# Kernel tuning notes

Measured on AMD Instinct MI355X. Metric: run time of the kernel, lower is better.

The kernel has to match this reference:

```python
import jax, jax.numpy as jnp
import numpy as np

N = 10000   # nodes
E = 160000  # edges (before self-loops)
IN = 77     # input feature dim
H = 4       # heads (layers 1,2)
C = 128     # per-head out channels


def setup_inputs() -> dict:
    key = jax.random.key(0)
    ks = jax.random.split(key, 16)
    p = lambda k, shape: (jax.random.normal(k, shape, jnp.float32) * 0.1)
    z = lambda n: jnp.zeros((n,), jnp.float32)
    return {
        "x": jax.random.normal(ks[0], (N, IN), jnp.float32),
        "edge_index": jax.random.randint(ks[1], (2, E), 0, N),
        # layer 1: 77 -> H*C
        "Wl1": p(ks[2], (H * C, IN)), "bl1": z(H * C),
        "Wr1": p(ks[3], (H * C, IN)), "br1": z(H * C),
        "att1": p(ks[4], (H, C)), "b1": z(H * C),
        # layer 2: H*C -> H*C
        "Wl2": p(ks[5], (H * C, H * C)), "bl2": z(H * C),
        "Wr2": p(ks[6], (H * C, H * C)), "br2": z(H * C),
        "att2": p(ks[7], (H, C)), "b2": z(H * C),
        # layer 3: H*C -> C (1 head)
        "Wl3": p(ks[8], (C, H * C)), "bl3": z(C),
        "Wr3": p(ks[9], (C, H * C)), "br3": z(C),
        "att3": p(ks[10], (1, C)), "b3": z(C),
    }


def _gatv2_layer(x, src, dst, Wl, bl, Wr, br, att, bias, heads, outc):
    """PyG GATv2Conv (eval mode, self-loops already in src/dst, concat=True)."""
    n = x.shape[0]
    xl = (x @ Wl.T + bl).reshape(n, heads, outc)  # source transform
    xr = (x @ Wr.T + br).reshape(n, heads, outc)  # target transform
    # edge-wise score: a^T LeakyReLU(xl[src] + xr[dst])
    e = jax.nn.leaky_relu(xl[src] + xr[dst], negative_slope=0.2)  # [E,H,C]
    logits = jnp.einsum('ehc,hc->eh', e, att)                      # [E,H]
    # segment softmax over edges grouped by destination node
    m = jax.lax.stop_gradient(jax.ops.segment_max(logits, dst, num_segments=n))
    ev = jnp.exp(logits - m[dst])
    denom = jax.ops.segment_sum(ev, dst, num_segments=n)
    alpha = ev / (denom[dst] + 1e-16)                              # [E,H]
    # scatter-add weighted messages
    out = jax.ops.segment_sum(xl[src] * alpha[:, :, None], dst, num_segments=n)
    return out.reshape(n, heads * outc) + bias


def reference(x, edge_index, Wl1, bl1, Wr1, br1, att1, b1,
              Wl2, bl2, Wr2, br2, att2, b2,
              Wl3, bl3, Wr3, br3, att3, b3):
    n = x.shape[0]
    loop = jnp.arange(n)
    src = jnp.concatenate([edge_index[0], loop])  # add self-loops (PyG default)
    dst = jnp.concatenate([edge_index[1], loop])
    h = jax.nn.elu(_gatv2_layer(x, src, dst, Wl1, bl1, Wr1, br1, att1, b1, H, C))
    h = jax.nn.elu(_gatv2_layer(h, src, dst, Wl2, bl2, Wr2, br2, att2, b2, H, C))
    return _gatv2_layer(h, src, dst, Wl3, bl3, Wr3, br3, att3, b3, 1, C)
```

## Files before the change

kernel.cpp:

```cpp
#include <hip/hip_runtime.h>
#include <hip/hip_bf16.h>
#include <math.h>

typedef __attribute__((ext_vector_type(8))) short short8;
typedef __attribute__((ext_vector_type(4))) float f32x4;
typedef __attribute__((ext_vector_type(2))) float f32x2;
typedef __attribute__((ext_vector_type(4))) unsigned int u32x4;

__device__ __forceinline__ float bf2f(unsigned short u) {
  union { unsigned int i; float f; } x; x.i = ((unsigned int)u) << 16; return x.f;
}

__device__ __forceinline__ f32x2 pk_add(f32x2 a, f32x2 b) {
  f32x2 d; asm("v_pk_add_f32 %0, %1, %2" : "=v"(d) : "v"(a), "v"(b)); return d;
}
__device__ __forceinline__ f32x2 pk_fma(f32x2 a, f32x2 b, f32x2 c) {
  f32x2 d; asm("v_pk_fma_f32 %0, %1, %2, %3" : "=v"(d) : "v"(a), "v"(b), "v"(c)); return d;
}
__device__ __forceinline__ f32x2 pk_abs(f32x2 a) {
  union { f32x2 f; unsigned int u[2]; } x; x.f = a;
  x.u[0] &= 0x7fffffffu; x.u[1] &= 0x7fffffffu;
  return x.f;
}
__device__ __forceinline__ f32x2 unpk(unsigned int w) {
  union { f32x2 f; unsigned int u[2]; } x;
  x.u[0] = w << 16;
  x.u[1] = w & 0xffff0000u;
  return x.f;
}

template <int CTRL>
__device__ __forceinline__ float dpp_add(float x) {
  int y = __builtin_amdgcn_update_dpp(0, __builtin_bit_cast(int, x), CTRL, 0xF, 0xF, true);
  return x + __builtin_bit_cast(float, y);
}
__device__ __forceinline__ float row16_sum(float p) {
  p = dpp_add<0xB1>(p);
  p = dpp_add<0x4E>(p);
  p = dpp_add<0x124>(p);
  p = dpp_add<0x128>(p);
  return p;
}

__device__ __forceinline__ void load_lds16(const void* g, void* l) {
  __builtin_amdgcn_global_load_lds(
      (const __attribute__((address_space(1))) unsigned int*)g,
      (__attribute__((address_space(3))) unsigned int*)l, 16, 0, 0);
}

__global__ __launch_bounds__(256) void gemm_mfma(
    const __hip_bfloat16* __restrict__ A, const __hip_bfloat16* __restrict__ B,
    const float* __restrict__ bl, const float* __restrict__ br, int halfN,
    __hip_bfloat16* __restrict__ out, int M, int K, int Nout) {
  __shared__ __hip_bfloat16 As[128 * 32];
  __shared__ __hip_bfloat16 Bs[128 * 32];
  int t = threadIdx.x;
  int w = t >> 6, l = t & 63;
  int lr = l & 15, lh = l >> 4;
  int wr = w >> 1, wc = w & 1;
  int m0 = blockIdx.y * 128, n0 = blockIdx.x * 128;
  f32x4 acc[4][4] = {};
  int nk = K >> 5;
  for (int ks = 0; ks < nk; ++ks) {
    int k0 = ks << 5;
#pragma unroll
    for (int p = 0; p < 2; ++p) {
      int c = p * 256 + t;
      int row = c >> 2, sub = c & 3;
      int gm = m0 + row; if (gm >= M) gm = M - 1;
      const __hip_bfloat16* gsrc = A + (size_t)gm * K + k0 + sub * 8;
      char* ldst = (char*)As + (size_t)(p * 256 + w * 64) * 16;
      load_lds16(gsrc, ldst);
    }
#pragma unroll
    for (int p = 0; p < 2; ++p) {
      int c = p * 256 + t;
      int row = c >> 2, sub = c & 3;
      const __hip_bfloat16* gsrc = B + (size_t)(n0 + row) * K + k0 + sub * 8;
      char* ldst = (char*)Bs + (size_t)(p * 256 + w * 64) * 16;
      load_lds16(gsrc, ldst);
    }
    __syncthreads();
    short8 af[4], bf[4];
#pragma unroll
    for (int mt = 0; mt < 4; ++mt)
      af[mt] = *(const short8*)(As + (size_t)(wr * 64 + mt * 16 + lr) * 32 + lh * 8);
#pragma unroll
    for (int nt = 0; nt < 4; ++nt)
      bf[nt] = *(const short8*)(Bs + (size_t)(wc * 64 + nt * 16 + lr) * 32 + lh * 8);
#pragma unroll
    for (int mt = 0; mt < 4; ++mt)
#pragma unroll
      for (int nt = 0; nt < 4; ++nt)
        acc[mt][nt] = __builtin_amdgcn_mfma_f32_16x16x32_bf16(af[mt], bf[nt], acc[mt][nt], 0, 0, 0);
    __syncthreads();
  }
#pragma unroll
  for (int mt = 0; mt < 4; ++mt) {
#pragma unroll
    for (int r = 0; r < 4; ++r) {
      int gm = m0 + wr * 64 + mt * 16 + lh * 4 + r;
      if (gm >= M) continue;
#pragma unroll
      for (int nt = 0; nt < 4; ++nt) {
        int gn = n0 + wc * 64 + nt * 16 + lr;
        float bv = (gn < halfN) ? bl[gn] : br[gn - halfN];
        out[(size_t)gm * Nout + gn] = __float2bfloat16(acc[mt][nt][r] + bv);
      }
    }
  }
}

struct CastSeg { const float* src; __hip_bfloat16* dst; int rows, K, Kp, row0, start; };
struct CastArgs { CastSeg s[7]; int total; };

__global__ __launch_bounds__(256) void k_prep(CastArgs A, const int* __restrict__ ei,
                                              int E, int N, int* __restrict__ deg) {
  int stride = gridDim.x * blockDim.x;
  int tid0 = blockIdx.x * blockDim.x + threadIdx.x;
  for (int i = tid0; i < A.total; i += stride) {
    int si = 0;
#pragma unroll
    for (int j = 1; j < 7; j++) if (i >= A.s[j].start) si = j;
    CastSeg sg = A.s[si];
    int li = i - sg.start;
    int r = li / sg.Kp, k = li - r * sg.Kp;
    float v = (k < sg.K) ? sg.src[(size_t)r * sg.K + k] : 0.f;
    sg.dst[(size_t)(sg.row0 + r) * sg.Kp + k] = __float2bfloat16(v);
  }
  int ET = E + N;
  for (int e = tid0; e < ET; e += stride) {
    int d = (e < E) ? ei[E + e] : (e - E);
    atomicAdd(&deg[d], 1);
  }
}

__global__ __launch_bounds__(256) void k_scan_perm(const int* __restrict__ deg, int N,
                                                   int* __restrict__ rp, int* __restrict__ cursor,
                                                   int* __restrict__ perm) {
  __shared__ int part[256];
  __shared__ int bcnt[64];
  __shared__ int boff[64];
  int t = threadIdx.x;
  int chunk = (N + 255) / 256;
  int lo = t * chunk;
  int hi = lo + chunk; if (hi > N) hi = N;
  int s = 0;
  for (int i = lo; i < hi; ++i) s += deg[i];
  part[t] = s;
  if (t < 64) bcnt[t] = 0;
  __syncthreads();
  for (int off = 1; off < 256; off <<= 1) {
    int x = (t >= off) ? part[t - off] : 0;
    __syncthreads();
    part[t] += x;
    __syncthreads();
  }
  int run = (t == 0) ? 0 : part[t - 1];
  for (int i = lo; i < hi; ++i) {
    rp[i] = run;
    cursor[i] = run;
    run += deg[i];
    int b = deg[i] < 63 ? deg[i] : 63;
    atomicAdd(&bcnt[b], 1);
  }
  if (t == 255) rp[N] = run;
  __syncthreads();
  if (t == 0) {
    int acc = 0;
    for (int b = 63; b >= 0; --b) { boff[b] = acc; acc += bcnt[b]; }
  }
  __syncthreads();
  for (int i = lo; i < hi; ++i) {
    int b = deg[i] < 63 ? deg[i] : 63;
    int pos = atomicAdd(&boff[b], 1);
    perm[pos] = i;
  }
}

__global__ void k_scatter(const int* __restrict__ ei, int E, int N,
                          int* __restrict__ cursor, int* __restrict__ srcs) {
  int e = blockIdx.x * blockDim.x + threadIdx.x;
  int ET = E + N;
  if (e >= ET) {
    if (e < ET + 64) srcs[e] = 0;
    return;
  }
  int s = (e < E) ? ei[e] : (e - E);
  int d = (e < E) ? ei[E + e] : (e - E);
  int pos = atomicAdd(&cursor[d], 1);
  srcs[pos] = s;
}

template <int CPL> struct VecSel;
template <> struct VecSel<8> { using T = short8; };
template <> struct VecSel<2> { using T = unsigned int; };

template <int HC, int Hn, int LDc, bool ELU, typename OutT>
__global__ __launch_bounds__(256) void k_edge_fused(
    const __hip_bfloat16* __restrict__ xl, const __hip_bfloat16* __restrict__ xr,
    const int* __restrict__ rp, const int* __restrict__ srcs,
    const int* __restrict__ perm,
    const float* __restrict__ att, const float* __restrict__ bias,
    int N, OutT* __restrict__ out) {
  const int CPL = HC / 64;
  const int NP = CPL / 2;
  using VecT = typename VecSel<CPL>::T;
  int lane = threadIdx.x & 63;
  int nw = (blockIdx.x * blockDim.x + threadIdx.x) >> 6;
  if (nw >= N) return;
  int n = __builtin_amdgcn_readfirstlane(perm[nw]);

  f32x2 a06[NP], a04[NP], xrv2[NP];
#pragma unroll
  for (int p = 0; p < NP; ++p) {
    float alo = att[lane * CPL + 2 * p], ahi = att[lane * CPL + 2 * p + 1];
    a06[p].x = 0.6f * alo; a06[p].y = 0.6f * ahi;
    a04[p].x = 0.4f * alo; a04[p].y = 0.4f * ahi;
  }
  {
    const unsigned int* xw = (const unsigned int*)(xr + (size_t)n * LDc + lane * CPL);
#pragma unroll
    for (int p = 0; p < NP; ++p) xrv2[p] = unpk(xw[p]);
  }

  int s0 = __builtin_amdgcn_readfirstlane(rp[n]);
  int s1 = __builtin_amdgcn_readfirstlane(rp[n + 1]);
  int len = s1 - s0;
  float sum = 0.f;
  f32x2 acc2[NP];
#pragma unroll
  for (int p = 0; p < NP; ++p) { acc2[p].x = 0.f; acc2[p].y = 0.f; }

  auto rowAt = [&](int s) -> VecT {
    return *(const VecT*)(xl + (size_t)s * LDc + lane * CPL);
  };
  auto proc = [&](VecT v) {
    unsigned int wv[NP];
    if constexpr (CPL == 8) {
      union { VecT s; u32x4 w; } u; u.s = v;
#pragma unroll
      for (int p = 0; p < NP; ++p) wv[p] = u.w[p];
    } else {
      wv[0] = (unsigned int)v;
    }
    f32x2 xv2[NP];
    f32x2 p2; p2.x = 0.f; p2.y = 0.f;
#pragma unroll
    for (int p = 0; p < NP; ++p) {
      xv2[p] = unpk(wv[p]);
      f32x2 s = pk_add(xv2[p], xrv2[p]);
      f32x2 sa = pk_abs(s);
      p2 = pk_fma(a06[p], s, p2);
      p2 = pk_fma(a04[p], sa, p2);
    }
    float pp = p2.x + p2.y;
    pp = row16_sum(pp);
    if constexpr (Hn == 1) {
      pp += __shfl_xor(pp, 16, 64);
      pp += __shfl_xor(pp, 32, 64);
    }
    float wgt = __expf(pp);
    sum += wgt;
    f32x2 wgt2; wgt2.x = wgt; wgt2.y = wgt;
#pragma unroll
    for (int p = 0; p < NP; ++p) acc2[p] = pk_fma(wgt2, xv2[p], acc2[p]);
  };

  VecT b0 = rowAt(srcs[s0]);
  VecT b1 = rowAt(srcs[s0 + 1]);
  int i = 0;
  for (; i + 1 < len; i += 2) {
    VecT n0 = rowAt(srcs[s0 + i + 2]);
    VecT n1 = rowAt(srcs[s0 + i + 3]);
    proc(b0);
    proc(b1);
    b0 = n0; b1 = n1;
  }
  if (i < len) proc(b0);

  float inv = 1.f / (sum + 1e-16f);
#pragma unroll
  for (int p = 0; p < NP; ++p) {
    float r0 = acc2[p].x * inv + bias[lane * CPL + 2 * p];
    float r1 = acc2[p].y * inv + bias[lane * CPL + 2 * p + 1];
    if (ELU) {
      r0 = r0 > 0.f ? r0 : expm1f(r0);
      r1 = r1 > 0.f ? r1 : expm1f(r1);
    }
    acc2[p].x = r0; acc2[p].y = r1;
  }
  if constexpr (sizeof(OutT) == 2) {
    short8 o;
#pragma unroll
    for (int p = 0; p < NP; ++p) {
      __hip_bfloat16 b0v = __float2bfloat16(acc2[p].x);
      __hip_bfloat16 b1v = __float2bfloat16(acc2[p].y);
      o[2 * p] = __builtin_bit_cast(short, b0v);
      o[2 * p + 1] = __builtin_bit_cast(short, b1v);
    }
    *(short8*)((__hip_bfloat16*)out + (size_t)n * HC + lane * CPL) = o;
  } else {
    f32x2 o; o.x = acc2[0].x; o.y = acc2[0].y;
    *(f32x2*)((float*)out + (size_t)n * HC + lane * 2) = o;
  }
}

extern "C" void kernel_launch(void* const* d_in, const int* in_sizes, int n_in,
                              void* d_out, int out_size, void* d_ws, size_t ws_size,
                              hipStream_t stream) {
  const int IN = 77, Kp1 = 96, Hh = 4, Cc = 128, HC = Hh * Cc;
  const int N = in_sizes[0] / IN;
  const int E = in_sizes[1] / 2;
  const int ET = E + N;

  const float* x   = (const float*)d_in[0];
  const int*   ei  = (const int*)d_in[1];
  const float* Wl1 = (const float*)d_in[2];  const float* bl1 = (const float*)d_in[3];
  const float* Wr1 = (const float*)d_in[4];  const float* br1 = (const float*)d_in[5];
  const float* att1= (const float*)d_in[6];  const float* b1  = (const float*)d_in[7];
  const float* Wl2 = (const float*)d_in[8];  const float* bl2 = (const float*)d_in[9];
  const float* Wr2 = (const float*)d_in[10]; const float* br2 = (const float*)d_in[11];
  const float* att2= (const float*)d_in[12]; const float* b2  = (const float*)d_in[13];
  const float* Wl3 = (const float*)d_in[14]; const float* bl3 = (const float*)d_in[15];
  const float* Wr3 = (const float*)d_in[16]; const float* br3 = (const float*)d_in[17];
  const float* att3= (const float*)d_in[18]; const float* b3  = (const float*)d_in[19];
  float* out = (float*)d_out;

  char* w = (char*)d_ws;
  size_t off = 0;
  auto alloc = [&](size_t bytes) -> void* {
    void* p = w + off;
    off += (bytes + 255) & ~(size_t)255;
    return p;
  };
  __hip_bfloat16* xlr = (__hip_bfloat16*)alloc((size_t)N * 2 * HC * 2);
  __hip_bfloat16* hb  = (__hip_bfloat16*)alloc((size_t)N * HC * 2);
  __hip_bfloat16* Wc1 = (__hip_bfloat16*)alloc((size_t)2 * HC * Kp1 * 2);
  __hip_bfloat16* Wc2 = (__hip_bfloat16*)alloc((size_t)2 * HC * HC * 2);
  __hip_bfloat16* Wc3 = (__hip_bfloat16*)alloc((size_t)2 * Cc * HC * 2);
  int*   deg    = (int*)alloc((size_t)N * 4);
  int*   rp     = (int*)alloc((size_t)(N + 1) * 4);
  int*   cursor = (int*)alloc((size_t)N * 4);
  int*   srcs   = (int*)alloc((size_t)(ET + 64) * 4);
  int*   perm   = (int*)alloc((size_t)N * 4);

  CastArgs CA;
  int cum = 0;
  auto seg = [&](int idx, const float* src, __hip_bfloat16* dst, int rows, int K, int Kp, int row0) {
    CA.s[idx] = {src, dst, rows, K, Kp, row0, cum};
    cum += rows * Kp;
  };
  seg(0, Wl1, Wc1, HC, IN, Kp1, 0);
  seg(1, Wr1, Wc1, HC, IN, Kp1, HC);
  seg(2, Wl2, Wc2, HC, HC, HC, 0);
  seg(3, Wr2, Wc2, HC, HC, HC, HC);
  seg(4, Wl3, Wc3, Cc, HC, HC, 0);
  seg(5, Wr3, Wc3, Cc, HC, HC, Cc);
  seg(6, x,   hb,  N,  IN, Kp1, 0);
  CA.total = cum;

  hipMemsetAsync(deg, 0, (size_t)N * 4, stream);
  k_prep<<<1024, 256, 0, stream>>>(CA, ei, E, N, deg);
  k_scan_perm<<<1, 256, 0, stream>>>(deg, N, rp, cursor, perm);
  k_scatter<<<(ET + 64 + 255) / 256, 256, 0, stream>>>(ei, E, N, cursor, srcs);

  int nodeBlocks = (N + 3) / 4;
  int mb = (N + 127) / 128;

  {
    dim3 g(2 * HC / 128, mb);
    gemm_mfma<<<g, 256, 0, stream>>>(hb, Wc1, bl1, br1, HC, xlr, N, Kp1, 2 * HC);
    k_edge_fused<512, 4, 1024, true, __hip_bfloat16><<<nodeBlocks, 256, 0, stream>>>(
        xlr, xlr + HC, rp, srcs, perm, att1, b1, N, hb);
  }
  {
    dim3 g(2 * HC / 128, mb);
    gemm_mfma<<<g, 256, 0, stream>>>(hb, Wc2, bl2, br2, HC, xlr, N, HC, 2 * HC);
    k_edge_fused<512, 4, 1024, true, __hip_bfloat16><<<nodeBlocks, 256, 0, stream>>>(
        xlr, xlr + HC, rp, srcs, perm, att2, b2, N, hb);
  }
  {
    dim3 g(2 * Cc / 128, mb);
    gemm_mfma<<<g, 256, 0, stream>>>(hb, Wc3, bl3, br3, Cc, xlr, N, HC, 2 * Cc);
    k_edge_fused<128, 1, 256, false, float><<<nodeBlocks, 256, 0, stream>>>(
        xlr, xlr + Cc, rp, srcs, perm, att3, b3, N, out);
  }
}
```

Baseline: 193.2 us.

## Split edge lists across wave halves/quarters to process multiple edges concurrently

Replaces the templated per-node edge kernel with two specialised versions. For the 4-head layers each half-wave handles half of a node's incoming edges with 16 channels per lane; for the single-head final layer each quarter-wave handles a quarter of the edges. Partial sums and softmax denominators are combined at the end with cross-lane shuffles. The aim is to raise memory-level parallelism on the neighbour gathers. The cost is extra reduction work, wider per-lane vectors that raise register pressure, and masked lanes when the edge counts are uneven.

```diff
diff --git a/kernel.cpp b/kernel.cpp
--- a/kernel.cpp
+++ b/kernel.cpp
@@ -6,10 +6,6 @@
 typedef __attribute__((ext_vector_type(4))) float f32x4;
 typedef __attribute__((ext_vector_type(2))) float f32x2;
 typedef __attribute__((ext_vector_type(4))) unsigned int u32x4;
-
-__device__ __forceinline__ float bf2f(unsigned short u) {
-  union { unsigned int i; float f; } x; x.i = ((unsigned int)u) << 16; return x.f;
-}
 
 __device__ __forceinline__ f32x2 pk_add(f32x2 a, f32x2 b) {
   f32x2 d; asm("v_pk_add_f32 %0, %1, %2" : "=v"(d) : "v"(a), "v"(b)); return d;
@@ -192,63 +188,162 @@
   srcs[pos] = s;
 }
 
-template <int CPL> struct VecSel;
-template <> struct VecSel<8> { using T = short8; };
-template <> struct VecSel<2> { using T = unsigned int; };
-
-template <int HC, int Hn, int LDc, bool ELU, typename OutT>
-__global__ __launch_bounds__(256) void k_edge_fused(
+__global__ __launch_bounds__(256) void k_edge2(
     const __hip_bfloat16* __restrict__ xl, const __hip_bfloat16* __restrict__ xr,
     const int* __restrict__ rp, const int* __restrict__ srcs,
-    const int* __restrict__ perm,
-    const float* __restrict__ att, const float* __restrict__ bias,
-    int N, OutT* __restrict__ out) {
-  const int CPL = HC / 64;
-  const int NP = CPL / 2;
-  using VecT = typename VecSel<CPL>::T;
+    const int* __restrict__ perm, const float* __restrict__ att,
+    const float* __restrict__ bias, int N, __hip_bfloat16* __restrict__ out) {
+  const int LD = 1024;
   int lane = threadIdx.x & 63;
+  int hl = lane & 31;
+  bool hi = lane >= 32;
   int nw = (blockIdx.x * blockDim.x + threadIdx.x) >> 6;
   if (nw >= N) return;
   int n = __builtin_amdgcn_readfirstlane(perm[nw]);
 
-  f32x2 a06[NP], a04[NP], xrv2[NP];
-#pragma unroll
-  for (int p = 0; p < NP; ++p) {
-    float alo = att[lane * CPL + 2 * p], ahi = att[lane * CPL + 2 * p + 1];
+  f32x2 a06[8], a04[8], xrv2[8];
+#pragma unroll
+  for (int p = 0; p < 8; ++p) {
+    float alo = att[hl * 16 + 2 * p], ahi = att[hl * 16 + 2 * p + 1];
     a06[p].x = 0.6f * alo; a06[p].y = 0.6f * ahi;
     a04[p].x = 0.4f * alo; a04[p].y = 0.4f * ahi;
   }
   {
-    const unsigned int* xw = (const unsigned int*)(xr + (size_t)n * LDc + lane * CPL);
-#pragma unroll
-    for (int p = 0; p < NP; ++p) xrv2[p] = unpk(xw[p]);
+    const unsigned int* xw = (const unsigned int*)(xr + (size_t)n * LD + hl * 16);
+#pragma unroll
+    for (int p = 0; p < 8; ++p) xrv2[p] = unpk(xw[p]);
   }
 
   int s0 = __builtin_amdgcn_readfirstlane(rp[n]);
   int s1 = __builtin_amdgcn_readfirstlane(rp[n + 1]);
   int len = s1 - s0;
+  int lenA = (len + 1) >> 1;
+  int lenB = len - lenA;
+  int iA = s0, iB = s0 + lenA;
+
   float sum = 0.f;
-  f32x2 acc2[NP];
-#pragma unroll
-  for (int p = 0; p < NP; ++p) { acc2[p].x = 0.f; acc2[p].y = 0.f; }
-
-  auto rowAt = [&](int s) -> VecT {
-    return *(const VecT*)(xl + (size_t)s * LDc + lane * CPL);
+  f32x2 acc2[8];
+#pragma unroll
+  for (int p = 0; p < 8; ++p) { acc2[p].x = 0.f; acc2[p].y = 0.f; }
+
+  auto rowPtr = [&](int sA, int sB) -> const u32x4* {
+    int s = hi ? sB : sA;
+    return (const u32x4*)(xl + (size_t)s * LD + hl * 16);
   };
-  auto proc = [&](VecT v) {
-    unsigned int wv[NP];
-    if constexpr (CPL == 8) {
-      union { VecT s; u32x4 w; } u; u.s = v;
-#pragma unroll
-      for (int p = 0; p < NP; ++p) wv[p] = u.w[p];
-    } else {
-      wv[0] = (unsigned int)v;
+
+  u32x4 curLo, curHi;
+  {
+    const u32x4* p = rowPtr(srcs[iA], srcs[iB]);
+    curLo = p[0]; curHi = p[1];
+  }
+  for (int t = 0; t < lenA; ++t) {
+    const u32x4* pn = rowPtr(srcs[iA + t + 1], srcs[iB + t + 1]);
+    u32x4 nLo = pn[0], nHi = pn[1];
+    f32x2 xv2[8], p2; p2.x = 0.f; p2.y = 0.f;
+#pragma unroll
+    for (int p = 0; p < 8; ++p) {
+      unsigned int wv = (p < 4) ? curLo[p & 3] : curHi[p & 3];
+      xv2[p] = unpk(wv);
+      f32x2 s = pk_add(xv2[p], xrv2[p]);
+      f32x2 sa = pk_abs(s);
+      p2 = pk_fma(a06[p], s, p2);
+      p2 = pk_fma(a04[p], sa, p2);
     }
-    f32x2 xv2[NP];
-    f32x2 p2; p2.x = 0.f; p2.y = 0.f;
-#pragma unroll
-    for (int p = 0; p < NP; ++p) {
-      xv2[p] = unpk(wv[p]);
+    float pp = p2.x + p2.y;
+    pp = dpp_add<0xB1>(pp);
+    pp = dpp_add<0x4E>(pp);
+    pp += __shfl_xor(pp, 4, 64);
+    float wgt = __expf(pp);
+    if (hi && t >= lenB) wgt = 0.f;
+    sum += wgt;
+    f32x2 w2; w2.x = wgt; w2.y = wgt;
+#pragma unroll
+    for (int p = 0; p < 8; ++p) acc2[p] = pk_fma(w2, xv2[p], acc2[p]);
+    curLo = nLo; curHi = nHi;
+  }
+
+  sum += __shfl_xor(sum, 32, 64);
+#pragma unroll
+  for (int p = 0; p < 8; ++p) {
+    f32x2 o;
+    o.x = __shfl_xor(acc2[p].x, 32, 64);
+    o.y = __shfl_xor(acc2[p].y, 32, 64);
+    acc2[p] = pk_add(acc2[p], o);
+  }
+  float inv = 1.f / (sum + 1e-16f);
+  int cbase = hl * 16 + (hi ? 8 : 0);
+  short8 o;
+#pragma unroll
+  for (int q = 0; q < 4; ++q) {
+    f32x2 v = hi ? acc2[4 + q] : acc2[q];
+    float r0 = v.x * inv + bias[cbase + 2 * q];
+    float r1 = v.y * inv + bias[cbase + 2 * q + 1];
+    r0 = r0 > 0.f ? r0 : expm1f(r0);
+    r1 = r1 > 0.f ? r1 : expm1f(r1);
+    __hip_bfloat16 b0 = __float2bfloat16(r0);
+    __hip_bfloat16 b1 = __float2bfloat16(r1);
+    o[2 * q] = __builtin_bit_cast(short, b0);
+    o[2 * q + 1] = __builtin_bit_cast(short, b1);
+  }
+  *(short8*)(out + (size_t)n * 512 + cbase) = o;
+}
+
+__global__ __launch_bounds__(256) void k_edge4(
+    const __hip_bfloat16* __restrict__ xl, const __hip_bfloat16* __restrict__ xr,
+    const int* __restrict__ rp, const int* __restrict__ srcs,
+    const int* __restrict__ perm, const float* __restrict__ att,
+    const float* __restrict__ bias, int N, float* __restrict__ out) {
+  const int LD = 256;
+  int lane = threadIdx.x & 63;
+  int hl = lane & 15;
+  int g = lane >> 4;
+  int nw = (blockIdx.x * blockDim.x + threadIdx.x) >> 6;
+  if (nw >= N) return;
+  int n = __builtin_amdgcn_readfirstlane(perm[nw]);
+
+  f32x2 a06[4], a04[4], xrv2[4];
+#pragma unroll
+  for (int p = 0; p < 4; ++p) {
+    float alo = att[hl * 8 + 2 * p], ahi = att[hl * 8 + 2 * p + 1];
+    a06[p].x = 0.6f * alo; a06[p].y = 0.6f * ahi;
+    a04[p].x = 0.4f * alo; a04[p].y = 0.4f * ahi;
+  }
+  {
+    const unsigned int* xw = (const unsigned int*)(xr + (size_t)n * LD + hl * 8);
+#pragma unroll
+    for (int p = 0; p < 4; ++p) xrv2[p] = unpk(xw[p]);
+  }
+
+  int s0 = __builtin_amdgcn_readfirstlane(rp[n]);
+  int s1 = __builtin_amdgcn_readfirstlane(rp[n + 1]);
+  int len = s1 - s0;
+  int base = len >> 2, rem = len & 3;
+  int l0 = base + (rem > 0 ? 1 : 0);
+  int l1 = base + (rem > 1 ? 1 : 0);
+  int l2 = base + (rem > 2 ? 1 : 0);
+  int st0 = 0, st1 = l0, st2 = l0 + l1, st3 = l0 + l1 + l2;
+  int lg = base + ((g < rem) ? 1 : 0);
+  int itmax = (len < 4) ? 1 : l0;
+  if (l0 == 0) itmax = 0;
+
+  float sum = 0.f;
+  f32x2 acc2[4];
+#pragma unroll
+  for (int p = 0; p < 4; ++p) { acc2[p].x = 0.f; acc2[p].y = 0.f; }
+
+  auto rowPtr = [&](int e0, int e1, int e2, int e3) -> const u32x4* {
+    int s = (g == 0) ? e0 : (g == 1) ? e1 : (g == 2) ? e2 : e3;
+    return (const u32x4*)(xl + (size_t)s * LD + hl * 8);
+  };
+
+  u32x4 cur = *rowPtr(srcs[s0 + st0], srcs[s0 + st1], srcs[s0 + st2], srcs[s0 + st3]);
+  for (int t = 0; t < itmax; ++t) {
+    u32x4 nxt = *rowPtr(srcs[s0 + st0 + t + 1], srcs[s0 + st1 + t + 1],
+                        srcs[s0 + st2 + t + 1], srcs[s0 + st3 + t + 1]);
+    f32x2 xv2[4], p2; p2.x = 0.f; p2.y = 0.f;
+#pragma unroll
+    for (int p = 0; p < 4; ++p) {
+      xv2[p] = unpk(cur[p]);
       f32x2 s = pk_add(xv2[p], xrv2[p]);
       f32x2 sa = pk_abs(s);
       p2 = pk_fma(a06[p], s, p2);
@@ -256,54 +351,30 @@
     }
     float pp = p2.x + p2.y;
     pp = row16_sum(pp);
-    if constexpr (Hn == 1) {
-      pp += __shfl_xor(pp, 16, 64);
-      pp += __shfl_xor(pp, 32, 64);
-    }
-    float wgt = __expf(pp);
+    float wgt = (t < lg) ? __expf(pp) : 0.f;
     sum += wgt;
-    f32x2 wgt2; wgt2.x = wgt; wgt2.y = wgt;
-#pragma unroll
-    for (int p = 0; p < NP; ++p) acc2[p] = pk_fma(wgt2, xv2[p], acc2[p]);
-  };
-
-  VecT b0 = rowAt(srcs[s0]);
-  VecT b1 = rowAt(srcs[s0 + 1]);
-  int i = 0;
-  for (; i + 1 < len; i += 2) {
-    VecT n0 = rowAt(srcs[s0 + i + 2]);
-    VecT n1 = rowAt(srcs[s0 + i + 3]);
-    proc(b0);
-    proc(b1);
-    b0 = n0; b1 = n1;
-  }
-  if (i < len) proc(b0);
-
+    f32x2 w2; w2.x = wgt; w2.y = wgt;
+#pragma unroll
+    for (int p = 0; p < 4; ++p) acc2[p] = pk_fma(w2, xv2[p], acc2[p]);
+    cur = nxt;
+  }
+
+  sum += __shfl_xor(sum, 16, 64);
+  sum += __shfl_xor(sum, 32, 64);
+#pragma unroll
+  for (int p = 0; p < 4; ++p) {
+    acc2[p].x += __shfl_xor(acc2[p].x, 16, 64);
+    acc2[p].y += __shfl_xor(acc2[p].y, 16, 64);
+    acc2[p].x += __shfl_xor(acc2[p].x, 32, 64);
+    acc2[p].y += __shfl_xor(acc2[p].y, 32, 64);
+  }
   float inv = 1.f / (sum + 1e-16f);
-#pragma unroll
-  for (int p = 0; p < NP; ++p) {
-    float r0 = acc2[p].x * inv + bias[lane * CPL + 2 * p];
-    float r1 = acc2[p].y * inv + bias[lane * CPL + 2 * p + 1];
-    if (ELU) {
-      r0 = r0 > 0.f ? r0 : expm1f(r0);
-      r1 = r1 > 0.f ? r1 : expm1f(r1);
-    }
-    acc2[p].x = r0; acc2[p].y = r1;
-  }
-  if constexpr (sizeof(OutT) == 2) {
-    short8 o;
-#pragma unroll
-    for (int p = 0; p < NP; ++p) {
-      __hip_bfloat16 b0v = __float2bfloat16(acc2[p].x);
-      __hip_bfloat16 b1v = __float2bfloat16(acc2[p].y);
-      o[2 * p] = __builtin_bit_cast(short, b0v);
-      o[2 * p + 1] = __builtin_bit_cast(short, b1v);
-    }
-    *(short8*)((__hip_bfloat16*)out + (size_t)n * HC + lane * CPL) = o;
-  } else {
-    f32x2 o; o.x = acc2[0].x; o.y = acc2[0].y;
-    *(f32x2*)((float*)out + (size_t)n * HC + lane * 2) = o;
-  }
+  f32x2 v = (g == 0) ? acc2[0] : (g == 1) ? acc2[1] : (g == 2) ? acc2[2] : acc2[3];
+  int cb = hl * 8 + 2 * g;
+  f32x2 r;
+  r.x = v.x * inv + bias[cb];
+  r.y = v.y * inv + bias[cb + 1];
+  *(f32x2*)(out + (size_t)n * 128 + cb) = r;
 }
 
 extern "C" void kernel_launch(void* const* d_in, const int* in_sizes, int n_in,
@@ -371,19 +442,16 @@
   {
     dim3 g(2 * HC / 128, mb);
     gemm_mfma<<<g, 256, 0, stream>>>(hb, Wc1, bl1, br1, HC, xlr, N, Kp1, 2 * HC);
-    k_edge_fused<512, 4, 1024, true, __hip_bfloat16><<<nodeBlocks, 256, 0, stream>>>(
-        xlr, xlr + HC, rp, srcs, perm, att1, b1, N, hb);
+    k_edge2<<<nodeBlocks, 256, 0, stream>>>(xlr, xlr + HC, rp, srcs, perm, att1, b1, N, hb);
   }
   {
     dim3 g(2 * HC / 128, mb);
     gemm_mfma<<<g, 256, 0, stream>>>(hb, Wc2, bl2, br2, HC, xlr, N, HC, 2 * HC);
-    k_edge_fused<512, 4, 1024, true, __hip_bfloat16><<<nodeBlocks, 256, 0, stream>>>(
-        xlr, xlr + HC, rp, srcs, perm, att2, b2, N, hb);
+    k_edge2<<<nodeBlocks, 256, 0, stream>>>(xlr, xlr + HC, rp, srcs, perm, att2, b2, N, hb);
   }
   {
     dim3 g(2 * Cc / 128, mb);
     gemm_mfma<<<g, 256, 0, stream>>>(hb, Wc3, bl3, br3, Cc, xlr, N, HC, 2 * Cc);
-    k_edge_fused<128, 1, 256, false, float><<<nodeBlocks, 256, 0, stream>>>(
-        xlr, xlr + Cc, rp, srcs, perm, att3, b3, N, out);
-  }
-}
+    k_edge4<<<nodeBlocks, 256, 0, stream>>>(xlr, xlr + Cc, rp, srcs, perm, att3, b3, N, out);
+  }
+}
```

New measurement: 194.5 us. No clear change (+0.7%).
